# Kernel tuning notes

Hardware: AMD Instinct MI355X
Metric: run time of the kernel (lower is better)

## Reference

```python
import math
import jax, jax.numpy as jnp
import numpy as np

N_LAYERS = 30
RC = 64        # residual_channels
N_MELS = 80
TED = 128      # time_emb_dim
CD = 256       # text_dim
B, T = 8, 8192
EPS = 1e-12    # F.normalize eps


def conv1d(x, w, b, dilation=1, padding=0):
    # x: [B,C,T], w: [O,I,K], b: [O]
    y = jax.lax.conv_general_dilated(
        x, w, window_strides=(1,), padding=[(padding, padding)],
        rhs_dilation=(dilation,), dimension_numbers=("NCH", "OIH", "NCH"))
    return y + b[None, :, None]


def sinusoidal_embedding(t, dim):
    half = dim // 2
    freqs = jnp.exp(jnp.arange(half, dtype=jnp.float32) * (-math.log(10000.0) / (half - 1)))
    ang = t.astype(jnp.float32)[:, None] * freqs[None, :]
    return jnp.concatenate([jnp.sin(ang), jnp.cos(ang)], axis=1)  # [B, dim]


def mish(x):
    return x * jnp.tanh(jax.nn.softplus(x))


def setup_inputs() -> dict:
    key = jax.random.key(0)
    ks = jax.random.split(key, 24)
    s = 0.05
    inp = {
        "x": jax.random.normal(ks[0], (B, 1, N_MELS, T), jnp.float32),
        "t": jax.random.randint(ks[1], (B,), 0, 1000),
        "c_emb": jax.random.normal(ks[2], (B, CD), jnp.float32),
        # input_proj: Conv1d(n_mels, RC, 1)
        "in_w": jax.random.normal(ks[3], (RC, N_MELS, 1), jnp.float32) * s,
        "in_b": jnp.zeros((RC,), jnp.float32),
        # time MLP: Linear(TED, 4*TED), Mish, Linear(4*TED, TED). torch weight [out,in]
        "te_w1": jax.random.normal(ks[4], (4 * TED, TED), jnp.float32) * s,
        "te_b1": jnp.zeros((4 * TED,), jnp.float32),
        "te_w2": jax.random.normal(ks[5], (TED, 4 * TED), jnp.float32) * s,
        "te_b2": jnp.zeros((TED,), jnp.float32),
        # per-layer stacked params
        "dconv_w": jax.random.normal(ks[6], (N_LAYERS, 2 * RC, RC, 3), jnp.float32) * s,
        "dconv_b": jnp.zeros((N_LAYERS, 2 * RC), jnp.float32),
        "tproj_w": jax.random.normal(ks[7], (N_LAYERS, 2 * RC, TED), jnp.float32) * s,
        "tproj_b": jnp.zeros((N_LAYERS, 2 * RC), jnp.float32),
        "cproj_w": jax.random.normal(ks[8], (N_LAYERS, 2 * RC, CD), jnp.float32) * s,
        "cproj_b": jnp.zeros((N_LAYERS, 2 * RC), jnp.float32),
        "rs_w": jax.random.normal(ks[9], (N_LAYERS, 2 * RC, RC, 1), jnp.float32) * s,
        "rs_b": jnp.zeros((N_LAYERS, 2 * RC), jnp.float32),
        "skip_w": jax.random.normal(ks[10], (RC, RC, 1), jnp.float32) * s,
        "skip_b": jnp.zeros((RC,), jnp.float32),
        "out_w": jax.random.normal(ks[11], (N_MELS, RC, 1), jnp.float32) * s,
        "out_b": jnp.zeros((N_MELS,), jnp.float32),
    }
    return inp


def reference(x, t, c_emb, in_w, in_b, te_w1, te_b1, te_w2, te_b2,
              dconv_w, dconv_b, tproj_w, tproj_b, cproj_w, cproj_b,
              rs_w, rs_b, skip_w, skip_b, out_w, out_b):
    h = x[:, 0]                                  # squeeze(1) -> [B, n_mels, T]
    h = conv1d(h, in_w, in_b)                    # [B, RC, T]
    te = sinusoidal_embedding(t, TED)
    te = mish(te @ te_w1.T + te_b1) @ te_w2.T + te_b2   # [B, TED]

    skips = jnp.zeros_like(conv1d(h, rs_w[0], rs_b[0])[:, :RC])  # [B, RC, T]
    skips = jnp.zeros((h.shape[0], RC, h.shape[2]), h.dtype)
    for i in range(N_LAYERS):
        dil = 2 ** (i % 10)
        g = conv1d(h, dconv_w[i], dconv_b[i], dilation=dil, padding=dil)  # [B, 2RC, T]
        tp = (te @ tproj_w[i].T + tproj_b[i])[:, :, None]                 # [B, 2RC, 1]
        tp = tp / jnp.maximum(jnp.abs(tp), EPS)      # F.normalize over size-1 dim
        cp = (c_emb @ cproj_w[i].T + cproj_b[i])[:, :, None]
        cp = cp / jnp.maximum(jnp.abs(cp), EPS)
        g = g + tp + cp
        gate, filt = g[:, :RC], g[:, RC:]            # chunk(2, dim=1)
        out = jnp.tanh(filt) * jax.nn.sigmoid(gate)
        rs = conv1d(out, rs_w[i], rs_b[i])           # [B, 2RC, T]
        res, skip = rs[:, :RC], rs[:, RC:]
        h = h + res * (1.0 / math.sqrt(2.0))
        skips = skips + skip

    y = skips / math.sqrt(N_LAYERS)
    y = jax.nn.relu(conv1d(y, skip_w, skip_b))
    y = conv1d(y, out_w, out_b)                      # [B, n_mels, T]
    return y[:, None]                                # unsqueeze(1)
```

## Files before the change

### kernel.cpp

```cpp
#include <hip/hip_runtime.h>
#include <hip/hip_bf16.h>
#include <math.h>

#define NL 30
#define NM 80
#define Bx 8
#define Tx 8192

typedef short short8 __attribute__((ext_vector_type(8)));
typedef float f32x4 __attribute__((ext_vector_type(4)));
typedef unsigned int u32x2 __attribute__((ext_vector_type(2)));
typedef unsigned int u32x4 __attribute__((ext_vector_type(4)));

__device__ __forceinline__ float bf2f(unsigned short u) {
    union { unsigned int u; float f; } v; v.u = ((unsigned int)u) << 16; return v.f;
}
__device__ __forceinline__ unsigned short f2bf(float f) {
    union { float f; unsigned int u; } v; v.f = f;
    unsigned int r = v.u + 0x7FFFu + ((v.u >> 16) & 1u);
    return (unsigned short)(r >> 16);
}

#if defined(__has_builtin)
#if __has_builtin(__builtin_amdgcn_global_load_lds)
#define HAS_GLL 1
#endif
#endif

__device__ __forceinline__ void gll16(const void* g, void* l) {
#ifdef HAS_GLL
    __builtin_amdgcn_global_load_lds(
        (const __attribute__((address_space(1))) void*)g,
        (__attribute__((address_space(3))) void*)l, 16, 0, 0);
#else
    int lane = threadIdx.x & 63;
    *(u32x4*)((char*)l + lane * 16) = *(const u32x4*)((const char*)g + lane * 16);
#endif
}

__global__ void te_kernel(const int* __restrict__ tin,
                          const float* __restrict__ w1, const float* __restrict__ b1,
                          const float* __restrict__ w2, const float* __restrict__ b2,
                          float* __restrict__ te_out) {
    __shared__ float emb[128];
    __shared__ float h1s[512];
    __shared__ float red[512];
    int b = blockIdx.x, tid = threadIdx.x;
    if (tid < 64) {
        float fr = expf(-(float)tid * (logf(10000.f) / 63.f));
        float ang = (float)tin[b] * fr;
        emb[tid] = sinf(ang);
        emb[tid + 64] = cosf(ang);
    }
    __syncthreads();
    float a = b1[tid];
    const float* wr = w1 + tid * 128;
    for (int k = 0; k < 128; ++k) a = fmaf(emb[k], wr[k], a);
    float sp = (a > 15.f) ? a : log1pf(expf(a));
    h1s[tid] = a * tanhf(sp);
    __syncthreads();
    int o = tid & 127, q = tid >> 7;
    float p = 0.f;
    const float* wr2 = w2 + o * 512 + q * 128;
    const float* hq = h1s + q * 128;
    for (int k = 0; k < 128; ++k) p = fmaf(hq[k], wr2[k], p);
    red[tid] = p;
    __syncthreads();
    if (q == 0)
        te_out[b * 128 + o] = b2[o] + red[o] + red[o + 128] + red[o + 256] + red[o + 384];
}

__global__ void gbias_kernel(const float* __restrict__ te,
                             const float* __restrict__ cemb,
                             const float* __restrict__ tpw, const float* __restrict__ tpb,
                             const float* __restrict__ cpw, const float* __restrict__ cpb,
                             const float* __restrict__ dcb,
                             float* __restrict__ gbias) {
    int l = blockIdx.x >> 3;
    int b = blockIdx.x & 7;
    int ch = threadIdx.x;
    float tp = tpb[l * 128 + ch];
    const float* wr = tpw + (size_t)(l * 128 + ch) * 128;
    const float* tb = te + b * 128;
    for (int k = 0; k < 128; ++k) tp = fmaf(tb[k], wr[k], tp);
    float s1 = tp / fmaxf(fabsf(tp), 1e-12f);
    float cp = cpb[l * 128 + ch];
    const float* wcp = cpw + (size_t)(l * 128 + ch) * 256;
    const float* cb = cemb + b * 256;
    for (int k = 0; k < 256; ++k) cp = fmaf(cb[k], wcp[k], cp);
    float s2 = cp / fmaxf(fabsf(cp), 1e-12f);
    gbias[(l * 8 + b) * 128 + ch] = dcb[l * 128 + ch] + s1 + s2;
}

__global__ void prep_kernel(const float* __restrict__ dconv_w, const float* __restrict__ rs_w,
                            const float* __restrict__ skip_w, const float* __restrict__ out_w,
                            unsigned short* __restrict__ wc2, unsigned short* __restrict__ wr2,
                            unsigned short* __restrict__ skw16, unsigned short* __restrict__ oww16) {
    int idx = blockIdx.x * 256 + threadIdx.x;
    const int totC = NL * 24576;
    const int totR = NL * 128 * 64;
    if (idx < totC) {
        int l = idx / 24576;
        int r = idx - l * 24576;
        int c = r >> 3;
        int e = r & 7;
        int row = c >> 3;
        int p = c & 7;
        int col16 = p ^ (row & 7);
        int ic = col16 * 8 + e;
        int tap = row >> 7;
        int oc = row & 127;
        wc2[idx] = f2bf(dconv_w[((size_t)(l * 128 + oc) * 64 + ic) * 3 + tap]);
    } else if (idx < totC + totR) {
        int j = idx - totC;
        int l = j / 8192;
        int r = j - l * 8192;
        int c = r >> 3;
        int e = r & 7;
        int row = c >> 3;
        int p = c & 7;
        int col16 = p ^ (row & 7);
        int ic = col16 * 8 + e;
        wr2[j] = f2bf(rs_w[(size_t)(l * 128 + row) * 64 + ic]);
    } else if (idx < totC + totR + 4096) {
        int j = idx - totC - totR;
        skw16[j] = f2bf(skip_w[j] * 0.18257418583505536f);
    } else if (idx < totC + totR + 4096 + 5120) {
        int j = idx - totC - totR - 4096;
        oww16[j] = f2bf(out_w[j]);
    }
}

__global__ void in_conv_kernel(const float* __restrict__ x, const float* __restrict__ w,
                               const float* __restrict__ bias, unsigned short* __restrict__ h0) {
    __shared__ float wT[NM][64];
    int tid = threadIdx.x;
    for (int i = tid; i < NM * 64; i += 256) {
        int m = i >> 6, c = i & 63;
        wT[m][c] = w[c * NM + m];
    }
    __syncthreads();
    int b = blockIdx.y;
    int t = blockIdx.x * 128 + (tid >> 1);
    int ch0 = (tid & 1) * 32;
    const float* xp = x + (size_t)b * NM * Tx + t;
    float acc[32];
    #pragma unroll
    for (int c = 0; c < 32; ++c) acc[c] = bias[ch0 + c];
    for (int m = 0; m < NM; ++m) {
        float xv = xp[(size_t)m * Tx];
        #pragma unroll
        for (int c = 0; c < 32; ++c) acc[c] = fmaf(xv, wT[m][ch0 + c], acc[c]);
    }
    unsigned short* hp = h0 + ((size_t)b * Tx + t) * 64 + ch0;
    #pragma unroll
    for (int c = 0; c < 32; c += 2) {
        unsigned int p = (unsigned int)f2bf(acc[c]) | ((unsigned int)f2bf(acc[c + 1]) << 16);
        *(unsigned int*)(hp + c) = p;
    }
}

__launch_bounds__(512, 2)
__global__ void layer_kernel(const unsigned short* __restrict__ h_in,
                             unsigned short* __restrict__ h_out,
                             float* __restrict__ skips,
                             const unsigned short* __restrict__ wc2,
                             const unsigned short* __restrict__ wr2,
                             const float* __restrict__ gbias,
                             const float* __restrict__ rsb,
                             int dil, int first) {
    __shared__ __align__(16) unsigned char lds[98304];
    unsigned char* ldsA = lds;
    unsigned char* ldsR = lds + 49152;
    unsigned char* ldsO = lds + 65536;

    int tid = threadIdx.x;
    int wid = tid >> 6, lane = tid & 63, lr = lane & 15, lq = lane >> 4;

    #pragma unroll
    for (int j = 0; j < 6; ++j) {
        int cbase = j * 512 + wid * 64;
        gll16(wc2 + (size_t)(cbase + lane) * 8, ldsA + cbase * 16);
    }
    #pragma unroll
    for (int j = 0; j < 2; ++j) {
        int cbase = j * 512 + wid * 64;
        gll16(wr2 + (size_t)(cbase + lane) * 8, ldsR + cbase * 16);
    }

    int bid = blockIdx.x;
    int wg = (bid & 7) * 32 + (bid >> 3);
    int b = wg >> 5;
    int t0 = ((wg & 31) << 8) + wid * 32;

    const unsigned short* hb = h_in + (size_t)b * Tx * 64;
    short8 bv[3][2][2];
    #pragma unroll
    for (int tap = 0; tap < 3; ++tap) {
        int toff = (tap - 1) * dil;
        #pragma unroll
        for (int nf = 0; nf < 2; ++nf) {
            int t = t0 + nf * 16 + lr + toff;
            bool v = ((unsigned)t < (unsigned)Tx);
            #pragma unroll
            for (int kc = 0; kc < 2; ++kc) {
                short8 z = {0, 0, 0, 0, 0, 0, 0, 0};
                if (v) z = *(const short8*)(hb + t * 64 + kc * 32 + lq * 8);
                bv[tap][nf][kc] = z;
            }
        }
    }

    f32x4 acc[8][2];
    #pragma unroll
    for (int mf = 0; mf < 8; ++mf) {
        f32x4 bias4 = *(const f32x4*)(gbias + b * 128 + mf * 16 + lq * 4);
        acc[mf][0] = bias4;
        acc[mf][1] = bias4;
    }
    __syncthreads();

    #pragma unroll
    for (int tap = 0; tap < 3; ++tap) {
        #pragma unroll
        for (int kc = 0; kc < 2; ++kc) {
            #pragma unroll
            for (int mf = 0; mf < 8; ++mf) {
                int row = tap * 128 + mf * 16 + lr;
                short8 af = *(const short8*)(ldsA + row * 128 + ((kc * 64 + lq * 16) ^ ((lr & 7) << 4)));
                acc[mf][0] = __builtin_amdgcn_mfma_f32_16x16x32_bf16(af, bv[tap][0][kc], acc[mf][0], 0, 0, 0);
                acc[mf][1] = __builtin_amdgcn_mfma_f32_16x16x32_bf16(af, bv[tap][1][kc], acc[mf][1], 0, 0, 0);
            }
        }
    }

    unsigned char* myO = ldsO + wid * 4096;
    #pragma unroll
    for (int mf = 0; mf < 4; ++mf) {
        #pragma unroll
        for (int nf = 0; nf < 2; ++nf) {
            int p = nf * 16 + lr;
            unsigned short ob[4];
            #pragma unroll
            for (int r = 0; r < 4; ++r) {
                float g = acc[mf][nf][r];
                float f = acc[mf + 4][nf][r];
                f = fminf(f, 15.f);
                g = fminf(g, 30.f);
                float ea = __builtin_amdgcn_exp2f(f * 2.8853900817779268f);
                float eb = __builtin_amdgcn_exp2f(g * 1.4426950408889634f);
                float num = (ea - 1.f) * eb;
                float den = (ea + 1.f) * (1.f + eb);
                ob[r] = f2bf(num * __builtin_amdgcn_rcpf(den));
            }
            u32x2 pk;
            pk[0] = (unsigned int)ob[0] | ((unsigned int)ob[1] << 16);
            pk[1] = (unsigned int)ob[2] | ((unsigned int)ob[3] << 16);
            *(u32x2*)(myO + p * 128 + ((mf * 32 + lq * 8) ^ ((p & 7) << 4))) = pk;
        }
    }

    u32x2 hold[2][4];
    f32x4 skold[2][4];
    #pragma unroll
    for (int nf = 0; nf < 2; ++nf) {
        int t = t0 + nf * 16 + lr;
        size_t base = ((size_t)b * Tx + t) * 64;
        #pragma unroll
        for (int mf = 0; mf < 4; ++mf) {
            hold[nf][mf] = *(const u32x2*)(h_in + base + mf * 16 + lq * 4);
            if (!first) skold[nf][mf] = *(const f32x4*)(skips + base + mf * 16 + lq * 4);
            else { skold[nf][mf][0] = 0.f; skold[nf][mf][1] = 0.f; skold[nf][mf][2] = 0.f; skold[nf][mf][3] = 0.f; }
        }
    }

    f32x4 racc[8][2];
    #pragma unroll
    for (int mf = 0; mf < 8; ++mf) {
        f32x4 rb4 = *(const f32x4*)(rsb + mf * 16 + lq * 4);
        racc[mf][0] = rb4;
        racc[mf][1] = rb4;
    }
    #pragma unroll
    for (int kc = 0; kc < 2; ++kc) {
        short8 ob2[2];
        #pragma unroll
        for (int nf = 0; nf < 2; ++nf) {
            int p = nf * 16 + lr;
            ob2[nf] = *(const short8*)(myO + p * 128 + ((kc * 64 + lq * 16) ^ ((p & 7) << 4)));
        }
        #pragma unroll
        for (int mf = 0; mf < 8; ++mf) {
            int row = mf * 16 + lr;
            short8 af = *(const short8*)(ldsR + row * 128 + ((kc * 64 + lq * 16) ^ ((lr & 7) << 4)));
            racc[mf][0] = __builtin_amdgcn_mfma_f32_16x16x32_bf16(af, ob2[0], racc[mf][0], 0, 0, 0);
            racc[mf][1] = __builtin_amdgcn_mfma_f32_16x16x32_bf16(af, ob2[1], racc[mf][1], 0, 0, 0);
        }
    }

    const float inv_s2 = 0.70710678118654752f;
    #pragma unroll
    for (int nf = 0; nf < 2; ++nf) {
        int t = t0 + nf * 16 + lr;
        size_t base = ((size_t)b * Tx + t) * 64;
        #pragma unroll
        for (int mf = 0; mf < 4; ++mf) {
            unsigned short* hp = (unsigned short*)&hold[nf][mf];
            unsigned short hnew[4];
            #pragma unroll
            for (int r = 0; r < 4; ++r)
                hnew[r] = f2bf(bf2f(hp[r]) + racc[mf][nf][r] * inv_s2);
            u32x2 hw;
            hw[0] = (unsigned int)hnew[0] | ((unsigned int)hnew[1] << 16);
            hw[1] = (unsigned int)hnew[2] | ((unsigned int)hnew[3] << 16);
            *(u32x2*)(h_out + base + mf * 16 + lq * 4) = hw;
            f32x4 sk = skold[nf][mf] + racc[mf + 4][nf];
            *(f32x4*)(skips + base + mf * 16 + lq * 4) = sk;
        }
    }
}

__launch_bounds__(256, 2)
__global__ void out_kernel(const float* __restrict__ skips,
                           const unsigned short* __restrict__ skw,
                           const float* __restrict__ skb,
                           const unsigned short* __restrict__ oww,
                           const float* __restrict__ obias,
                           float* __restrict__ y) {
    __shared__ __align__(16) unsigned char ldsY[16384];
    int tid = threadIdx.x;
    int wid = tid >> 6;
    int lane = tid & 63;
    int lr = lane & 15;
    int lq = lane >> 4;

    int bid = blockIdx.x;
    int wg = (bid & 7) * 64 + (bid >> 3);
    int P0 = wg * 128 + wid * 32;
    int b = P0 >> 13;
    int t0 = P0 & 8191;

    short8 A1[4][2];
    #pragma unroll
    for (int mf = 0; mf < 4; ++mf)
        #pragma unroll
        for (int kc = 0; kc < 2; ++kc)
            A1[mf][kc] = *(const short8*)(skw + (mf * 16 + lr) * 64 + kc * 32 + lq * 8);

    short8 Bs[2][2];
    #pragma unroll
    for (int nf = 0; nf < 2; ++nf) {
        const float* sp = skips + ((size_t)P0 + nf * 16 + lr) * 64;
        #pragma unroll
        for (int kc = 0; kc < 2; ++kc) {
            f32x4 u = *(const f32x4*)(sp + kc * 32 + lq * 8);
            f32x4 v = *(const f32x4*)(sp + kc * 32 + lq * 8 + 4);
            short8 z;
            #pragma unroll
            for (int r = 0; r < 4; ++r) {
                z[r] = (short)f2bf(u[r]);
                z[r + 4] = (short)f2bf(v[r]);
            }
            Bs[nf][kc] = z;
        }
    }

    f32x4 acc1[4][2];
    #pragma unroll
    for (int mf = 0; mf < 4; ++mf) {
        f32x4 bb = *(const f32x4*)(skb + mf * 16 + lq * 4);
        acc1[mf][0] = bb;
        acc1[mf][1] = bb;
    }
    #pragma unroll
    for (int kc = 0; kc < 2; ++kc)
        #pragma unroll
        for (int mf = 0; mf < 4; ++mf) {
            acc1[mf][0] = __builtin_amdgcn_mfma_f32_16x16x32_bf16(A1[mf][kc], Bs[0][kc], acc1[mf][0], 0, 0, 0);
            acc1[mf][1] = __builtin_amdgcn_mfma_f32_16x16x32_bf16(A1[mf][kc], Bs[1][kc], acc1[mf][1], 0, 0, 0);
        }

    unsigned char* myY = ldsY + wid * 4096;
    #pragma unroll
    for (int mf = 0; mf < 4; ++mf)
        #pragma unroll
        for (int nf = 0; nf < 2; ++nf) {
            int p = nf * 16 + lr;
            unsigned short ob[4];
            #pragma unroll
            for (int r = 0; r < 4; ++r)
                ob[r] = f2bf(fmaxf(acc1[mf][nf][r], 0.f));
            u32x2 pk;
            pk[0] = (unsigned int)ob[0] | ((unsigned int)ob[1] << 16);
            pk[1] = (unsigned int)ob[2] | ((unsigned int)ob[3] << 16);
            *(u32x2*)(myY + p * 128 + ((mf * 32 + lq * 8) ^ ((p & 7) << 4))) = pk;
        }

    short8 B2[2][2];
    #pragma unroll
    for (int nf = 0; nf < 2; ++nf) {
        int p = nf * 16 + lr;
        #pragma unroll
        for (int kc = 0; kc < 2; ++kc)
            B2[nf][kc] = *(const short8*)(myY + p * 128 + ((kc * 64 + lq * 16) ^ ((p & 7) << 4)));
    }
    f32x4 acc2[5][2];
    #pragma unroll
    for (int mf = 0; mf < 5; ++mf) {
        f32x4 bb = *(const f32x4*)(obias + mf * 16 + lq * 4);
        acc2[mf][0] = bb;
        acc2[mf][1] = bb;
    }
    #pragma unroll
    for (int kc = 0; kc < 2; ++kc)
        #pragma unroll
        for (int mf = 0; mf < 5; ++mf) {
            short8 A2 = *(const short8*)(oww + (mf * 16 + lr) * 64 + kc * 32 + lq * 8);
            acc2[mf][0] = __builtin_amdgcn_mfma_f32_16x16x32_bf16(A2, B2[0][kc], acc2[mf][0], 0, 0, 0);
            acc2[mf][1] = __builtin_amdgcn_mfma_f32_16x16x32_bf16(A2, B2[1][kc], acc2[mf][1], 0, 0, 0);
        }

    #pragma unroll
    for (int mf = 0; mf < 5; ++mf)
        #pragma unroll
        for (int nf = 0; nf < 2; ++nf) {
            int t = t0 + nf * 16 + lr;
            #pragma unroll
            for (int r = 0; r < 4; ++r) {
                int m = mf * 16 + lq * 4 + r;
                y[((size_t)b * NM + m) * Tx + t] = acc2[mf][nf][r];
            }
        }
}

extern "C" void kernel_launch(void* const* d_in, const int* in_sizes, int n_in,
                              void* d_out, int out_size, void* d_ws, size_t ws_size,
                              hipStream_t stream) {
    const float* x       = (const float*)d_in[0];
    const int*   tin     = (const int*)d_in[1];
    const float* c_emb   = (const float*)d_in[2];
    const float* in_w    = (const float*)d_in[3];
    const float* in_b    = (const float*)d_in[4];
    const float* te_w1   = (const float*)d_in[5];
    const float* te_b1   = (const float*)d_in[6];
    const float* te_w2   = (const float*)d_in[7];
    const float* te_b2   = (const float*)d_in[8];
    const float* dconv_w = (const float*)d_in[9];
    const float* dconv_b = (const float*)d_in[10];
    const float* tproj_w = (const float*)d_in[11];
    const float* tproj_b = (const float*)d_in[12];
    const float* cproj_w = (const float*)d_in[13];
    const float* cproj_b = (const float*)d_in[14];
    const float* rs_w    = (const float*)d_in[15];
    const float* rs_b    = (const float*)d_in[16];
    const float* skip_w  = (const float*)d_in[17];
    const float* skip_b  = (const float*)d_in[18];
    const float* out_w   = (const float*)d_in[19];
    const float* out_b   = (const float*)d_in[20];

    char* ws = (char*)d_ws;
    float* te_buf         = (float*)(ws + 0);
    float* gbias          = (float*)(ws + 4096);
    unsigned short* skw16 = (unsigned short*)(ws + 126976);
    unsigned short* oww16 = (unsigned short*)(ws + 135168);
    unsigned short* wc2   = (unsigned short*)(ws + 145408);
    unsigned short* wr2   = (unsigned short*)(ws + 1619968);
    unsigned short* h0    = (unsigned short*)(ws + 2111488);
    unsigned short* h1    = (unsigned short*)(ws + 10500096);
    float* skips          = (float*)(ws + 18888704);

    te_kernel<<<8, 512, 0, stream>>>(tin, te_w1, te_b1, te_w2, te_b2, te_buf);
    gbias_kernel<<<240, 128, 0, stream>>>(te_buf, c_emb, tproj_w, tproj_b,
                                          cproj_w, cproj_b, dconv_b, gbias);
    prep_kernel<<<3876, 256, 0, stream>>>(dconv_w, rs_w, skip_w, out_w,
                                          wc2, wr2, skw16, oww16);
    in_conv_kernel<<<dim3(64, 8), 256, 0, stream>>>(x, in_w, in_b, h0);

    unsigned short* hin = h0;
    unsigned short* hout = h1;
    for (int i = 0; i < NL; ++i) {
        int dil = 1 << (i % 10);
        layer_kernel<<<256, 512, 0, stream>>>(hin, hout, skips,
                                              wc2 + (size_t)i * 24576,
                                              wr2 + (size_t)i * 8192,
                                              gbias + (size_t)i * 1024,
                                              rs_b + (size_t)i * 128,
                                              dil, i == 0 ? 1 : 0);
        unsigned short* tmp = hin; hin = hout; hout = tmp;
    }
    out_kernel<<<512, 256, 0, stream>>>(skips, skw16, skip_b, oww16, out_b,
                                        (float*)d_out);
}
```

Measured before the change: 590.1 us.

## Halve per-wave time tile in layer kernel and parallelize gbias dot products

The layer kernel now gives each wave 16 time steps instead of 32 and launches 512 workgroups instead of 256, with a smaller LDS footprint and a launch bound that asks for four blocks per CU. The goal is more workgroups and higher occupancy across the GPU's CUs. In exchange, each block reloads the same layer weights into LDS, doubling that traffic per layer. Separately, the gbias kernel switches from one thread per channel running a serial dot product to a wave-per-channel reduction with coalesced weight reads and shuffles.

```diff
diff --git a/kernel.cpp b/kernel.cpp
--- a/kernel.cpp
+++ b/kernel.cpp
@@ -78,18 +78,33 @@
                              float* __restrict__ gbias) {
     int l = blockIdx.x >> 3;
     int b = blockIdx.x & 7;
-    int ch = threadIdx.x;
-    float tp = tpb[l * 128 + ch];
-    const float* wr = tpw + (size_t)(l * 128 + ch) * 128;
-    const float* tb = te + b * 128;
-    for (int k = 0; k < 128; ++k) tp = fmaf(tb[k], wr[k], tp);
-    float s1 = tp / fmaxf(fabsf(tp), 1e-12f);
-    float cp = cpb[l * 128 + ch];
-    const float* wcp = cpw + (size_t)(l * 128 + ch) * 256;
-    const float* cb = cemb + b * 256;
-    for (int k = 0; k < 256; ++k) cp = fmaf(cb[k], wcp[k], cp);
-    float s2 = cp / fmaxf(fabsf(cp), 1e-12f);
-    gbias[(l * 8 + b) * 128 + ch] = dcb[l * 128 + ch] + s1 + s2;
+    int tid = threadIdx.x, wid = tid >> 6, lane = tid & 63;
+    float te0 = te[b * 128 + lane];
+    float te1 = te[b * 128 + 64 + lane];
+    float ce0 = cemb[b * 256 + lane];
+    float ce1 = cemb[b * 256 + 64 + lane];
+    float ce2 = cemb[b * 256 + 128 + lane];
+    float ce3 = cemb[b * 256 + 192 + lane];
+    #pragma unroll 4
+    for (int i = 0; i < 16; ++i) {
+        int ch = i * 8 + wid;
+        const float* wr = tpw + (size_t)(l * 128 + ch) * 128;
+        float s = te0 * wr[lane] + te1 * wr[lane + 64];
+        const float* wc = cpw + (size_t)(l * 128 + ch) * 256;
+        float sc = ce0 * wc[lane] + ce1 * wc[lane + 64] + ce2 * wc[lane + 128] + ce3 * wc[lane + 192];
+        #pragma unroll
+        for (int off = 32; off >= 1; off >>= 1) {
+            s += __shfl_xor(s, off, 64);
+            sc += __shfl_xor(sc, off, 64);
+        }
+        if (lane == 0) {
+            float tp = tpb[l * 128 + ch] + s;
+            float cp = cpb[l * 128 + ch] + sc;
+            float s1 = tp / fmaxf(fabsf(tp), 1e-12f);
+            float s2 = cp / fmaxf(fabsf(cp), 1e-12f);
+            gbias[(l * 8 + b) * 128 + ch] = dcb[l * 128 + ch] + s1 + s2;
+        }
+    }
 }
 
 __global__ void prep_kernel(const float* __restrict__ dconv_w, const float* __restrict__ rs_w,
@@ -160,7 +175,7 @@
     }
 }
 
-__launch_bounds__(512, 2)
+__launch_bounds__(512, 4)
 __global__ void layer_kernel(const unsigned short* __restrict__ h_in,
                              unsigned short* __restrict__ h_out,
                              float* __restrict__ skips,
@@ -169,7 +184,7 @@
                              const float* __restrict__ gbias,
                              const float* __restrict__ rsb,
                              int dil, int first) {
-    __shared__ __align__(16) unsigned char lds[98304];
+    __shared__ __align__(16) unsigned char lds[81920];
     unsigned char* ldsA = lds;
     unsigned char* ldsR = lds + 49152;
     unsigned char* ldsO = lds + 65536;
@@ -189,35 +204,29 @@
     }
 
     int bid = blockIdx.x;
-    int wg = (bid & 7) * 32 + (bid >> 3);
-    int b = wg >> 5;
-    int t0 = ((wg & 31) << 8) + wid * 32;
+    int wg = (bid & 7) * 64 + (bid >> 3);
+    int b = wg >> 6;
+    int t0 = ((wg & 63) << 7) + wid * 16;
 
     const unsigned short* hb = h_in + (size_t)b * Tx * 64;
-    short8 bv[3][2][2];
+    short8 bv[3][2];
     #pragma unroll
     for (int tap = 0; tap < 3; ++tap) {
         int toff = (tap - 1) * dil;
-        #pragma unroll
-        for (int nf = 0; nf < 2; ++nf) {
-            int t = t0 + nf * 16 + lr + toff;
-            bool v = ((unsigned)t < (unsigned)Tx);
-            #pragma unroll
-            for (int kc = 0; kc < 2; ++kc) {
-                short8 z = {0, 0, 0, 0, 0, 0, 0, 0};
-                if (v) z = *(const short8*)(hb + t * 64 + kc * 32 + lq * 8);
-                bv[tap][nf][kc] = z;
-            }
-        }
-    }
-
-    f32x4 acc[8][2];
-    #pragma unroll
-    for (int mf = 0; mf < 8; ++mf) {
-        f32x4 bias4 = *(const f32x4*)(gbias + b * 128 + mf * 16 + lq * 4);
-        acc[mf][0] = bias4;
-        acc[mf][1] = bias4;
-    }
+        int t = t0 + lr + toff;
+        bool v = ((unsigned)t < (unsigned)Tx);
+        #pragma unroll
+        for (int kc = 0; kc < 2; ++kc) {
+            short8 z = {0, 0, 0, 0, 0, 0, 0, 0};
+            if (v) z = *(const short8*)(hb + t * 64 + kc * 32 + lq * 8);
+            bv[tap][kc] = z;
+        }
+    }
+
+    f32x4 acc[8];
+    #pragma unroll
+    for (int mf = 0; mf < 8; ++mf)
+        acc[mf] = *(const f32x4*)(gbias + b * 128 + mf * 16 + lq * 4);
     __syncthreads();
 
     #pragma unroll
@@ -228,95 +237,75 @@
             for (int mf = 0; mf < 8; ++mf) {
                 int row = tap * 128 + mf * 16 + lr;
                 short8 af = *(const short8*)(ldsA + row * 128 + ((kc * 64 + lq * 16) ^ ((lr & 7) << 4)));
-                acc[mf][0] = __builtin_amdgcn_mfma_f32_16x16x32_bf16(af, bv[tap][0][kc], acc[mf][0], 0, 0, 0);
-                acc[mf][1] = __builtin_amdgcn_mfma_f32_16x16x32_bf16(af, bv[tap][1][kc], acc[mf][1], 0, 0, 0);
+                acc[mf] = __builtin_amdgcn_mfma_f32_16x16x32_bf16(af, bv[tap][kc], acc[mf], 0, 0, 0);
             }
         }
     }
 
-    unsigned char* myO = ldsO + wid * 4096;
+    unsigned char* myO = ldsO + wid * 2048;
     #pragma unroll
     for (int mf = 0; mf < 4; ++mf) {
-        #pragma unroll
-        for (int nf = 0; nf < 2; ++nf) {
-            int p = nf * 16 + lr;
-            unsigned short ob[4];
-            #pragma unroll
-            for (int r = 0; r < 4; ++r) {
-                float g = acc[mf][nf][r];
-                float f = acc[mf + 4][nf][r];
-                f = fminf(f, 15.f);
-                g = fminf(g, 30.f);
-                float ea = __builtin_amdgcn_exp2f(f * 2.8853900817779268f);
-                float eb = __builtin_amdgcn_exp2f(g * 1.4426950408889634f);
-                float num = (ea - 1.f) * eb;
-                float den = (ea + 1.f) * (1.f + eb);
-                ob[r] = f2bf(num * __builtin_amdgcn_rcpf(den));
-            }
-            u32x2 pk;
-            pk[0] = (unsigned int)ob[0] | ((unsigned int)ob[1] << 16);
-            pk[1] = (unsigned int)ob[2] | ((unsigned int)ob[3] << 16);
-            *(u32x2*)(myO + p * 128 + ((mf * 32 + lq * 8) ^ ((p & 7) << 4))) = pk;
-        }
-    }
-
-    u32x2 hold[2][4];
-    f32x4 skold[2][4];
-    #pragma unroll
-    for (int nf = 0; nf < 2; ++nf) {
-        int t = t0 + nf * 16 + lr;
-        size_t base = ((size_t)b * Tx + t) * 64;
-        #pragma unroll
-        for (int mf = 0; mf < 4; ++mf) {
-            hold[nf][mf] = *(const u32x2*)(h_in + base + mf * 16 + lq * 4);
-            if (!first) skold[nf][mf] = *(const f32x4*)(skips + base + mf * 16 + lq * 4);
-            else { skold[nf][mf][0] = 0.f; skold[nf][mf][1] = 0.f; skold[nf][mf][2] = 0.f; skold[nf][mf][3] = 0.f; }
-        }
-    }
-
-    f32x4 racc[8][2];
-    #pragma unroll
-    for (int mf = 0; mf < 8; ++mf) {
-        f32x4 rb4 = *(const f32x4*)(rsb + mf * 16 + lq * 4);
-        racc[mf][0] = rb4;
-        racc[mf][1] = rb4;
-    }
+        int p = lr;
+        unsigned short ob[4];
+        #pragma unroll
+        for (int r = 0; r < 4; ++r) {
+            float g = acc[mf][r];
+            float f = acc[mf + 4][r];
+            f = fminf(f, 15.f);
+            g = fminf(g, 30.f);
+            float ea = __builtin_amdgcn_exp2f(f * 2.8853900817779268f);
+            float eb = __builtin_amdgcn_exp2f(g * 1.4426950408889634f);
+            float num = (ea - 1.f) * eb;
+            float den = (ea + 1.f) * (1.f + eb);
+            ob[r] = f2bf(num * __builtin_amdgcn_rcpf(den));
+        }
+        u32x2 pk;
+        pk[0] = (unsigned int)ob[0] | ((unsigned int)ob[1] << 16);
+        pk[1] = (unsigned int)ob[2] | ((unsigned int)ob[3] << 16);
+        *(u32x2*)(myO + p * 128 + ((mf * 32 + lq * 8) ^ ((p & 7) << 4))) = pk;
+    }
+
+    int te_ = t0 + lr;
+    size_t base = ((size_t)b * Tx + te_) * 64;
+    u32x2 hold[4];
+    f32x4 skold[4];
+    #pragma unroll
+    for (int mf = 0; mf < 4; ++mf) {
+        hold[mf] = *(const u32x2*)(h_in + base + mf * 16 + lq * 4);
+        if (!first) skold[mf] = *(const f32x4*)(skips + base + mf * 16 + lq * 4);
+        else { skold[mf][0] = 0.f; skold[mf][1] = 0.f; skold[mf][2] = 0.f; skold[mf][3] = 0.f; }
+    }
+
+    f32x4 racc[8];
+    #pragma unroll
+    for (int mf = 0; mf < 8; ++mf)
+        racc[mf] = *(const f32x4*)(rsb + mf * 16 + lq * 4);
     #pragma unroll
     for (int kc = 0; kc < 2; ++kc) {
-        short8 ob2[2];
-        #pragma unroll
-        for (int nf = 0; nf < 2; ++nf) {
-            int p = nf * 16 + lr;
-            ob2[nf] = *(const short8*)(myO + p * 128 + ((kc * 64 + lq * 16) ^ ((p & 7) << 4)));
-        }
+        int p = lr;
+        short8 ov = *(const short8*)(myO + p * 128 + ((kc * 64 + lq * 16) ^ ((p & 7) << 4)));
         #pragma unroll
         for (int mf = 0; mf < 8; ++mf) {
             int row = mf * 16 + lr;
             short8 af = *(const short8*)(ldsR + row * 128 + ((kc * 64 + lq * 16) ^ ((lr & 7) << 4)));
-            racc[mf][0] = __builtin_amdgcn_mfma_f32_16x16x32_bf16(af, ob2[0], racc[mf][0], 0, 0, 0);
-            racc[mf][1] = __builtin_amdgcn_mfma_f32_16x16x32_bf16(af, ob2[1], racc[mf][1], 0, 0, 0);
+            racc[mf] = __builtin_amdgcn_mfma_f32_16x16x32_bf16(af, ov, racc[mf], 0, 0, 0);
         }
     }
 
     const float inv_s2 = 0.70710678118654752f;
     #pragma unroll
-    for (int nf = 0; nf < 2; ++nf) {
-        int t = t0 + nf * 16 + lr;
-        size_t base = ((size_t)b * Tx + t) * 64;
-        #pragma unroll
-        for (int mf = 0; mf < 4; ++mf) {
-            unsigned short* hp = (unsigned short*)&hold[nf][mf];
-            unsigned short hnew[4];
-            #pragma unroll
-            for (int r = 0; r < 4; ++r)
-                hnew[r] = f2bf(bf2f(hp[r]) + racc[mf][nf][r] * inv_s2);
-            u32x2 hw;
-            hw[0] = (unsigned int)hnew[0] | ((unsigned int)hnew[1] << 16);
-            hw[1] = (unsigned int)hnew[2] | ((unsigned int)hnew[3] << 16);
-            *(u32x2*)(h_out + base + mf * 16 + lq * 4) = hw;
-            f32x4 sk = skold[nf][mf] + racc[mf + 4][nf];
-            *(f32x4*)(skips + base + mf * 16 + lq * 4) = sk;
-        }
+    for (int mf = 0; mf < 4; ++mf) {
+        unsigned short* hp = (unsigned short*)&hold[mf];
+        unsigned short hnew[4];
+        #pragma unroll
+        for (int r = 0; r < 4; ++r)
+            hnew[r] = f2bf(bf2f(hp[r]) + racc[mf][r] * inv_s2);
+        u32x2 hw;
+        hw[0] = (unsigned int)hnew[0] | ((unsigned int)hnew[1] << 16);
+        hw[1] = (unsigned int)hnew[2] | ((unsigned int)hnew[3] << 16);
+        *(u32x2*)(h_out + base + mf * 16 + lq * 4) = hw;
+        f32x4 sk = skold[mf] + racc[mf + 4];
+        *(f32x4*)(skips + base + mf * 16 + lq * 4) = sk;
     }
 }
 
@@ -470,7 +459,7 @@
     float* skips          = (float*)(ws + 18888704);
 
     te_kernel<<<8, 512, 0, stream>>>(tin, te_w1, te_b1, te_w2, te_b2, te_buf);
-    gbias_kernel<<<240, 128, 0, stream>>>(te_buf, c_emb, tproj_w, tproj_b,
+    gbias_kernel<<<240, 512, 0, stream>>>(te_buf, c_emb, tproj_w, tproj_b,
                                           cproj_w, cproj_b, dconv_b, gbias);
     prep_kernel<<<3876, 256, 0, stream>>>(dconv_w, rs_w, skip_w, out_w,
                                           wc2, wr2, skw16, oww16);
@@ -480,7 +469,7 @@
     unsigned short* hout = h1;
     for (int i = 0; i < NL; ++i) {
         int dil = 1 << (i % 10);
-        layer_kernel<<<256, 512, 0, stream>>>(hin, hout, skips,
+        layer_kernel<<<512, 512, 0, stream>>>(hin, hout, skips,
                                               wc2 + (size_t)i * 24576,
                                               wr2 + (size_t)i * 8192,
                                               gbias + (size_t)i * 1024,
```

New measurement: 558.8 us. -5.3%, faster.
